# Performance work log

Hardware: AMD Instinct MI355X
Metric: run time of the kernel (lower is better)

Reference implementation:

```python
import jax, jax.numpy as jnp
import numpy as np

B, N, C, H = 2, 2048, 768, 12
D = C // H            # head_dim = 64
SCALE = D ** -0.5
QMAX_8 = 127.0        # int8 symmetric weights/activations (BIT_TYPE_W / BIT_TYPE_A)
LOG_QMAX = 15.0       # uint4 log-domain softmax (BIT_TYPE_S)


def setup_inputs() -> dict:
    key = jax.random.key(0)
    k0, k1, k2 = jax.random.split(key, 3)
    x = jax.random.normal(k0, (B, N, C), jnp.float32)
    w_qkv = jax.random.normal(k1, (3 * C, C), jnp.float32) * 0.02
    b_qkv = jnp.zeros((3 * C,), jnp.float32)
    w_out = jax.random.normal(k2, (C, C), jnp.float32) * 0.02
    b_out = jnp.zeros((C,), jnp.float32)
    return {"x": x, "w_qkv": w_qkv, "b_qkv": b_qkv, "w_out": w_out, "b_out": b_out}


def fake_quant_sym(t):
    """Symmetric per-tensor int8 fake-quantize (quantize->dequantize), STE for grads."""
    s = jnp.max(jnp.abs(t)) / QMAX_8 + 1e-8
    deq = jnp.clip(jnp.round(t / s), -QMAX_8, QMAX_8) * s
    return t + jax.lax.stop_gradient(deq - t)


def log_int_softmax(attn):
    """Log-int-softmax: softmax then 4-bit log2 quantization, attn_q = 2^{-round(-log2 p)}."""
    p = jax.nn.softmax(attn, axis=-1)
    lg = jnp.clip(jnp.round(-jnp.log2(jnp.maximum(p, 2.0 ** -24))), 0.0, LOG_QMAX)
    q = jnp.exp2(-lg)
    return p + jax.lax.stop_gradient(q - p)


def reference(x, w_qkv, b_qkv, w_out, b_out):
    # QLinear: fake-quantized weight GEMM
    qkv = x @ fake_quant_sym(w_qkv).T + b_qkv            # [B,N,3C]
    qkv = fake_quant_sym(qkv)                            # qact_qkv
    qkv = qkv.reshape(B, N, 3, H, D).transpose(2, 0, 3, 1, 4)  # [3,B,H,N,D]
    q, k, v = qkv[0], qkv[1], qkv[2]
    attn = jnp.einsum("bhnd,bhmd->bhnm", q, k) * SCALE   # [B,H,N,N]
    attn = fake_quant_sym(attn)                          # qact_attn
    p = log_int_softmax(attn)
    o = jnp.einsum("bhnm,bhmd->bhnd", p, v)              # [B,H,N,D]
    o = o.transpose(0, 2, 1, 3).reshape(B, N, C)
    out = o @ fake_quant_sym(w_out).T + b_out            # out_proj (QLinear)
    out = fake_quant_sym(out)                            # qact_out
    return out
```

## Files before the change

kernel.cpp:

```cpp
#include <hip/hip_runtime.h>

#define NB 2
#define NN 2048
#define NC 768
#define NH 12
#define ND 64
#define ROWS (NB * NN)
#define K3C (3 * NC)
#define NHEADS (NB * NH)
#define ATTN_SCALE 0.125f

typedef __attribute__((ext_vector_type(8))) short s16x8;
typedef __attribute__((ext_vector_type(4))) float f32x4;

__device__ __forceinline__ float qsc(const unsigned* u) {
    return __uint_as_float(*u) / 127.0f + 1e-8f;
}
__device__ __forceinline__ float fq(float t, float s) {
    return fminf(fmaxf(rintf(t / s), -127.0f), 127.0f) * s;
}
__device__ __forceinline__ float qcode(float t, float s) {
    return fminf(fmaxf(rintf(t / s), -127.0f), 127.0f);
}
__device__ __forceinline__ short bfbits(float f) {
    return (short)(__float_as_uint(f) >> 16);
}
__device__ __forceinline__ ushort bf_rne(float x) {
    unsigned u = __float_as_uint(x);
    return (ushort)((u + 0x7fffu + ((u >> 16) & 1u)) >> 16);
}

__global__ __launch_bounds__(256) void maxabs_kernel(const float* __restrict__ x,
                                                     long long n, unsigned* out) {
    float m = 0.0f;
    long long stride4 = (long long)gridDim.x * blockDim.x * 4;
    for (long long j = ((long long)blockIdx.x * blockDim.x + threadIdx.x) * 4; j < n; j += stride4) {
        float4 v = *(const float4*)(x + j);
        m = fmaxf(m, fmaxf(fmaxf(fabsf(v.x), fabsf(v.y)), fmaxf(fabsf(v.z), fabsf(v.w))));
    }
    for (int off = 32; off > 0; off >>= 1) m = fmaxf(m, __shfl_down(m, off, 64));
    __shared__ float sm[4];
    int lane = threadIdx.x & 63, w = threadIdx.x >> 6;
    if (lane == 0) sm[w] = m;
    __syncthreads();
    if (threadIdx.x == 0) {
        float mm = fmaxf(fmaxf(sm[0], sm[1]), fmaxf(sm[2], sm[3]));
        atomicMax(out, __float_as_uint(mm));
    }
}

__global__ __launch_bounds__(256) void quant_kernel(const float* in, float* out,
                                                    long long n, const unsigned* umax) {
    float s = qsc(umax);
    long long stride4 = (long long)gridDim.x * blockDim.x * 4;
    for (long long j = ((long long)blockIdx.x * blockDim.x + threadIdx.x) * 4; j < n; j += stride4) {
        float4 v = *(const float4*)(in + j);
        v.x = fq(v.x, s); v.y = fq(v.y, s); v.z = fq(v.z, s); v.w = fq(v.w, s);
        *(float4*)(out + j) = v;
    }
}

__global__ __launch_bounds__(256) void quantcodes_kernel(const float* __restrict__ in,
                                                         ushort* __restrict__ codes,
                                                         long long n,
                                                         const unsigned* __restrict__ umax) {
    float s = qsc(umax);
    long long stride8 = (long long)gridDim.x * blockDim.x * 8;
    for (long long j = ((long long)blockIdx.x * blockDim.x + threadIdx.x) * 8; j < n; j += stride8) {
        float4 a = *(const float4*)(in + j);
        float4 b = *(const float4*)(in + j + 4);
        s16x8 o;
        o[0] = bfbits(qcode(a.x, s)); o[1] = bfbits(qcode(a.y, s));
        o[2] = bfbits(qcode(a.z, s)); o[3] = bfbits(qcode(a.w, s));
        o[4] = bfbits(qcode(b.x, s)); o[5] = bfbits(qcode(b.y, s));
        o[6] = bfbits(qcode(b.z, s)); o[7] = bfbits(qcode(b.w, s));
        *(s16x8*)(codes + j) = o;
    }
}

__global__ __launch_bounds__(256) void split3_kernel(const float* __restrict__ in,
                                                     ushort* __restrict__ xs,
                                                     long long n) {
    long long stride8 = (long long)gridDim.x * blockDim.x * 8;
    for (long long j = ((long long)blockIdx.x * blockDim.x + threadIdx.x) * 8; j < n; j += stride8) {
        long long row = j / NC, col = j % NC;
        s16x8 h, m, l;
#pragma unroll
        for (int i = 0; i < 8; i += 4) {
            float4 v = *(const float4*)(in + j + i);
            float vv[4] = {v.x, v.y, v.z, v.w};
#pragma unroll
            for (int t = 0; t < 4; ++t) {
                ushort hb = bf_rne(vv[t]);
                float hf = __uint_as_float(((unsigned)hb) << 16);
                float r1 = vv[t] - hf;
                ushort mb = bf_rne(r1);
                float mf = __uint_as_float(((unsigned)mb) << 16);
                h[i + t] = (short)hb;
                m[i + t] = (short)mb;
                l[i + t] = (short)bf_rne(r1 - mf);
            }
        }
        ushort* dst = xs + row * (3 * NC) + col;
        *(s16x8*)(dst) = h;
        *(s16x8*)(dst + NC) = m;
        *(s16x8*)(dst + 2 * NC) = l;
    }
}

__global__ __launch_bounds__(256) void gemm3_mfma_kernel(const ushort* __restrict__ As,
                                                         const ushort* __restrict__ Bc,
                                                         const float* __restrict__ bias,
                                                         float* __restrict__ Cm, int Nn,
                                                         const unsigned* __restrict__ uB) {
    __shared__ ushort ah[128 * 64], am[128 * 64], al[128 * 64], bs[128 * 64];
    const float sB = qsc(uB);
    const int tid = threadIdx.x, l = tid & 63, w = tid >> 6;
    const int row0 = blockIdx.y * 128, col0 = blockIdx.x * 128;
    const int wr = w >> 1, wc = w & 1;
    f32x4 acc[4][4];
#pragma unroll
    for (int m = 0; m < 4; ++m)
#pragma unroll
        for (int n = 0; n < 4; ++n) acc[m][n] = (f32x4){0.f, 0.f, 0.f, 0.f};

    const int sr = tid >> 1, sh = (tid & 1) << 5;
    const int su = sh >> 3, s7 = sr & 7;

    for (int k0 = 0; k0 < NC; k0 += 64) {
        __syncthreads();
        {
            const ushort* ph = As + (size_t)(row0 + sr) * (3 * NC) + k0 + sh;
            ushort* dsts[3] = {ah + sr * 64, am + sr * 64, al + sr * 64};
#pragma unroll
            for (int pl = 0; pl < 3; ++pl) {
                const ushort* p = ph + pl * NC;
                s16x8 t0 = *(const s16x8*)(p),      t1 = *(const s16x8*)(p + 8);
                s16x8 t2 = *(const s16x8*)(p + 16), t3 = *(const s16x8*)(p + 24);
                ushort* d = dsts[pl];
                *(s16x8*)(d + (((su | 0) ^ s7) << 3)) = t0;
                *(s16x8*)(d + (((su | 1) ^ s7) << 3)) = t1;
                *(s16x8*)(d + (((su | 2) ^ s7) << 3)) = t2;
                *(s16x8*)(d + (((su | 3) ^ s7) << 3)) = t3;
            }
            const ushort* pb = Bc + (size_t)(col0 + sr) * NC + k0 + sh;
            s16x8 b0 = *(const s16x8*)(pb),      b1 = *(const s16x8*)(pb + 8);
            s16x8 b2 = *(const s16x8*)(pb + 16), b3 = *(const s16x8*)(pb + 24);
            ushort* brow = bs + sr * 64;
            *(s16x8*)(brow + (((su | 0) ^ s7) << 3)) = b0;
            *(s16x8*)(brow + (((su | 1) ^ s7) << 3)) = b1;
            *(s16x8*)(brow + (((su | 2) ^ s7) << 3)) = b2;
            *(s16x8*)(brow + (((su | 3) ^ s7) << 3)) = b3;
        }
        __syncthreads();
#pragma unroll
        for (int ks = 0; ks < 2; ++ks) {
            s16x8 bf[4];
#pragma unroll
            for (int n = 0; n < 4; ++n) {
                int br = wc * 64 + n * 16 + (l & 15);
                bf[n] = *(s16x8*)(bs + br * 64 + ((((ks << 2) + (l >> 4)) ^ (br & 7)) << 3));
            }
#pragma unroll
            for (int m = 0; m < 4; ++m) {
                int ar = wr * 64 + m * 16 + (l & 15);
                int ao = ar * 64 + ((((ks << 2) + (l >> 4)) ^ (ar & 7)) << 3);
                s16x8 af = *(s16x8*)(ah + ao);
                s16x8 mf_ = *(s16x8*)(am + ao);
                s16x8 ef = *(s16x8*)(al + ao);
#pragma unroll
                for (int n = 0; n < 4; ++n) {
                    acc[m][n] = __builtin_amdgcn_mfma_f32_16x16x32_bf16(af, bf[n], acc[m][n], 0, 0, 0);
                    acc[m][n] = __builtin_amdgcn_mfma_f32_16x16x32_bf16(mf_, bf[n], acc[m][n], 0, 0, 0);
                    acc[m][n] = __builtin_amdgcn_mfma_f32_16x16x32_bf16(ef, bf[n], acc[m][n], 0, 0, 0);
                }
            }
        }
    }
#pragma unroll
    for (int n = 0; n < 4; ++n) {
        int col = col0 + wc * 64 + n * 16 + (l & 15);
        float bv = bias[col];
#pragma unroll
        for (int m = 0; m < 4; ++m) {
            int grow = row0 + wr * 64 + m * 16 + ((l >> 4) << 2);
#pragma unroll
            for (int r = 0; r < 4; ++r)
                Cm[(size_t)(grow + r) * Nn + col] = fmaf(sB, acc[m][n][r], bv);
        }
    }
}

__device__ __forceinline__ void stage_k_tile(const ushort* __restrict__ src,
                                             ushort* lds, int tid) {
    int row = tid >> 2, u0 = (tid & 3) << 1, r7 = row & 7;
    const ushort* p = src + (size_t)row * K3C + (u0 << 3);
    s16x8 t0 = *(const s16x8*)(p);
    s16x8 t1 = *(const s16x8*)(p + 8);
    *(s16x8*)(lds + row * 64 + ((u0 ^ r7) << 3)) = t0;
    *(s16x8*)(lds + row * 64 + (((u0 | 1) ^ r7) << 3)) = t1;
}

__device__ __forceinline__ void stage_vT_tile(const ushort* __restrict__ src,
                                              ushort* lds, int tid) {
    int d = tid >> 2, j0 = (tid & 3) << 4;
    const ushort* p = src + (size_t)j0 * K3C + d;
    s16x8 a, b;
#pragma unroll
    for (int jj = 0; jj < 8; ++jj) a[jj] = (short)p[(size_t)jj * K3C];
#pragma unroll
    for (int jj = 0; jj < 8; ++jj) b[jj] = (short)p[(size_t)(8 + jj) * K3C];
    int u0 = j0 >> 3, d7 = d & 7;
    *(s16x8*)(lds + d * 64 + ((u0 ^ d7) << 3)) = a;
    *(s16x8*)(lds + d * 64 + (((u0 | 1) ^ d7) << 3)) = b;
}

__global__ __launch_bounds__(256) void attn_maxdot_kernel(const ushort* __restrict__ codes,
                                                          unsigned* __restrict__ umaxdot) {
    __shared__ ushort kt[64 * 64];
    __shared__ float red[4];
    int bh = blockIdx.y, b = bh / NH, h = bh % NH;
    int i0 = blockIdx.x * 64;
    int tid = threadIdx.x, l = tid & 63, w = tid >> 6;

    const ushort* qp = codes + (size_t)(b * NN + i0 + w * 16 + (l & 15)) * K3C + h * ND + ((l >> 4) << 3);
    s16x8 qf0 = *(const s16x8*)(qp);
    s16x8 qf1 = *(const s16x8*)(qp + 32);

    const ushort* kbase = codes + (size_t)(b * NN) * K3C + NC + h * ND;
    float md = 0.0f;
    for (int st = 0; st < NN / 64; ++st) {
        __syncthreads();
        stage_k_tile(kbase + (size_t)st * 64 * K3C, kt, tid);
        __syncthreads();
#pragma unroll
        for (int jt = 0; jt < 4; ++jt) {
            int row = (jt << 4) + (l & 15);
            f32x4 acc = {0.f, 0.f, 0.f, 0.f};
            s16x8 kf0 = *(s16x8*)(kt + row * 64 + ((((l >> 4)    ) ^ (row & 7)) << 3));
            s16x8 kf1 = *(s16x8*)(kt + row * 64 + ((((l >> 4) + 4) ^ (row & 7)) << 3));
            acc = __builtin_amdgcn_mfma_f32_16x16x32_bf16(qf0, kf0, acc, 0, 0, 0);
            acc = __builtin_amdgcn_mfma_f32_16x16x32_bf16(qf1, kf1, acc, 0, 0, 0);
#pragma unroll
            for (int r = 0; r < 4; ++r) md = fmaxf(md, fabsf(acc[r]));
        }
    }
    for (int m = 1; m < 64; m <<= 1) md = fmaxf(md, __shfl_xor(md, m, 64));
    if (l == 0) red[w] = md;
    __syncthreads();
    if (tid == 0)
        atomicMax(umaxdot, __float_as_uint(fmaxf(fmaxf(red[0], red[1]), fmaxf(red[2], red[3]))));
}

__global__ __launch_bounds__(256) void attn_fused_kernel(const ushort* __restrict__ codes,
                                                         const unsigned* __restrict__ uq,
                                                         const unsigned* __restrict__ umaxdot,
                                                         float* __restrict__ O) {
    __shared__ ushort kt[64 * 64];
    __shared__ ushort vt[64 * 64];
    __shared__ ushort ps[4][16 * 64];
    int bh = blockIdx.y, b = bh / NH, h = bh % NH;
    int i0 = blockIdx.x * 64;
    int tid = threadIdx.x, l = tid & 63, w = tid >> 6;
    float s = qsc(uq);
    float c = s * s * ATTN_SCALE;
    float sa = __uint_as_float(*umaxdot) * c / 127.0f + 1e-8f;
    float rr = c / sa;
    float kk = sa * 1.44269504088896340736f;

    const ushort* qp = codes + (size_t)(b * NN + i0 + w * 16 + (l & 15)) * K3C + h * ND + ((l >> 4) << 3);
    s16x8 qf0 = *(const s16x8*)(qp);
    s16x8 qf1 = *(const s16x8*)(qp + 32);

    const ushort* kbase = codes + (size_t)(b * NN) * K3C + NC + h * ND;
    const ushort* vbase = codes + (size_t)(b * NN) * K3C + 2 * NC + h * ND;

    float U[4] = {0.f, 0.f, 0.f, 0.f};
    for (int st = 0; st < NN / 64; ++st) {
        __syncthreads();
        stage_k_tile(kbase + (size_t)st * 64 * K3C, kt, tid);
        __syncthreads();
#pragma unroll
        for (int jt = 0; jt < 4; ++jt) {
            int row = (jt << 4) + (l & 15);
            f32x4 acc = {0.f, 0.f, 0.f, 0.f};
            s16x8 kf0 = *(s16x8*)(kt + row * 64 + ((((l >> 4)    ) ^ (row & 7)) << 3));
            s16x8 kf1 = *(s16x8*)(kt + row * 64 + ((((l >> 4) + 4) ^ (row & 7)) << 3));
            acc = __builtin_amdgcn_mfma_f32_16x16x32_bf16(qf0, kf0, acc, 0, 0, 0);
            acc = __builtin_amdgcn_mfma_f32_16x16x32_bf16(qf1, kf1, acc, 0, 0, 0);
#pragma unroll
            for (int r = 0; r < 4; ++r) {
                float m = rintf(acc[r] * rr);
                U[r] += exp2f(kk * m);
            }
        }
    }
#pragma unroll
    for (int r = 0; r < 4; ++r) {
        for (int msk = 1; msk < 16; msk <<= 1) U[r] += __shfl_xor(U[r], msk, 64);
    }
    float lu[4];
#pragma unroll
    for (int r = 0; r < 4; ++r) lu[r] = log2f(U[r]);

    f32x4 oacc[4];
#pragma unroll
    for (int dt = 0; dt < 4; ++dt) oacc[dt] = (f32x4){0.f, 0.f, 0.f, 0.f};
    ushort* myps = (ushort*)ps[w];
    for (int st = 0; st < NN / 64; ++st) {
        __syncthreads();
        stage_k_tile(kbase + (size_t)st * 64 * K3C, kt, tid);
        stage_vT_tile(vbase + (size_t)st * 64 * K3C, vt, tid);
        __syncthreads();
#pragma unroll
        for (int jt = 0; jt < 4; ++jt) {
            int row = (jt << 4) + (l & 15);
            f32x4 acc = {0.f, 0.f, 0.f, 0.f};
            s16x8 kf0 = *(s16x8*)(kt + row * 64 + ((((l >> 4)    ) ^ (row & 7)) << 3));
            s16x8 kf1 = *(s16x8*)(kt + row * 64 + ((((l >> 4) + 4) ^ (row & 7)) << 3));
            acc = __builtin_amdgcn_mfma_f32_16x16x32_bf16(qf0, kf0, acc, 0, 0, 0);
            acc = __builtin_amdgcn_mfma_f32_16x16x32_bf16(qf1, kf1, acc, 0, 0, 0);
#pragma unroll
            for (int r = 0; r < 4; ++r) {
                float m = rintf(acc[r] * rr);
                float tt = lu[r] - kk * m;
                float lg = fminf(fmaxf(rintf(tt), 0.0f), 15.0f);
                int lgi = (int)lg;
                ushort pbits = (ushort)((127 - lgi) << 7);
                int prow = ((l >> 4) << 2) + r;
                int j = (jt << 4) + (l & 15);
                int g = ((j >> 3) ^ (prow & 7)) ^ ((prow >> 3) << 2);
                myps[prow * 64 + (g << 3) + (j & 7)] = pbits;
            }
        }
#pragma unroll
        for (int kc = 0; kc < 2; ++kc) {
            int prow = l & 15;
            int gA = (((kc << 2) + (l >> 4)) ^ (prow & 7)) ^ ((prow >> 3) << 2);
            s16x8 pf = *(s16x8*)(myps + prow * 64 + (gA << 3));
#pragma unroll
            for (int dt = 0; dt < 4; ++dt) {
                int drow = (dt << 4) + (l & 15);
                s16x8 vf = *(s16x8*)(vt + drow * 64 + ((((kc << 2) + (l >> 4)) ^ (drow & 7)) << 3));
                oacc[dt] = __builtin_amdgcn_mfma_f32_16x16x32_bf16(pf, vf, oacc[dt], 0, 0, 0);
            }
        }
    }
#pragma unroll
    for (int dt = 0; dt < 4; ++dt)
#pragma unroll
        for (int r = 0; r < 4; ++r) {
            int orow = i0 + w * 16 + ((l >> 4) << 2) + r;
            O[(size_t)(b * NN + orow) * NC + h * ND + (dt << 4) + (l & 15)] = s * oacc[dt][r];
        }
}

extern "C" void kernel_launch(void* const* d_in, const int* in_sizes, int n_in,
                              void* d_out, int out_size, void* d_ws, size_t ws_size,
                              hipStream_t stream) {
    const float* x      = (const float*)d_in[0];
    const float* w_qkv  = (const float*)d_in[1];
    const float* b_qkv  = (const float*)d_in[2];
    const float* w_out  = (const float*)d_in[3];
    const float* b_out  = (const float*)d_in[4];
    float* out = (float*)d_out;

    char* ws = (char*)d_ws;
    unsigned* u = (unsigned*)ws;
    const size_t qkvB = (size_t)ROWS * K3C * 4;
    float*  qkv     = (float*)(ws + 256);
    float*  out_tmp = (float*)(ws + 256);
    ushort* woc     = (ushort*)(ws + 256 + 16 * 1024 * 1024);
    char*   codesRg = ws + 256 + qkvB;
    ushort* codes   = (ushort*)codesRg;
    ushort* xsplit  = (ushort*)codesRg;
    ushort* wqc     = (ushort*)d_out;

    hipMemsetAsync(u, 0, 64, stream);

    maxabs_kernel<<<512, 256, 0, stream>>>(w_qkv, (long long)K3C * NC, u + 0);
    maxabs_kernel<<<512, 256, 0, stream>>>(w_out, (long long)NC * NC, u + 1);
    quantcodes_kernel<<<512, 256, 0, stream>>>(w_qkv, wqc, (long long)K3C * NC, u + 0);

    split3_kernel<<<1024, 256, 0, stream>>>(x, xsplit, (long long)ROWS * NC);
    gemm3_mfma_kernel<<<dim3(K3C / 128, ROWS / 128), 256, 0, stream>>>(xsplit, wqc, b_qkv,
                                                                       qkv, K3C, u + 0);
    maxabs_kernel<<<1024, 256, 0, stream>>>(qkv, (long long)ROWS * K3C, u + 2);
    quantcodes_kernel<<<2048, 256, 0, stream>>>(qkv, codes, (long long)ROWS * K3C, u + 2);
    quantcodes_kernel<<<256, 256, 0, stream>>>(w_out, woc, (long long)NC * NC, u + 1);

    attn_maxdot_kernel<<<dim3(NN / 64, NHEADS), 256, 0, stream>>>(codes, u + 3);
    attn_fused_kernel<<<dim3(NN / 64, NHEADS), 256, 0, stream>>>(codes, u + 2, u + 3, out);

    split3_kernel<<<1024, 256, 0, stream>>>(out, xsplit, (long long)ROWS * NC);
    gemm3_mfma_kernel<<<dim3(NC / 128, ROWS / 128), 256, 0, stream>>>(xsplit, woc, b_out,
                                                                      out_tmp, NC, u + 1);
    maxabs_kernel<<<1024, 256, 0, stream>>>(out_tmp, (long long)ROWS * NC, u + 4);
    quant_kernel<<<1024, 256, 0, stream>>>(out_tmp, out, (long long)ROWS * NC, u + 4);
}
```

Baseline: 424.2 us.

## Fuse absmax into GEMM epilogue and transpose attention MFMA operands

Folds the per-tensor absmax reduction into the GEMM epilogue with wave shuffles and an atomicMax, which removes two full maxabs passes over the qkv and output tensors. The attention kernels swap the MFMA operand order so each lane holds a single query row's scores. That makes the softmax row sum a single scalar reduced with two shuffles, and the packed log-quantized probabilities are written with 8-byte LDS stores instead of scalar ones. V staging now uses coalesced vector global loads followed by scattered scalar LDS transposed writes, in place of strided global loads.

```diff
diff --git a/kernel.cpp b/kernel.cpp
--- a/kernel.cpp
+++ b/kernel.cpp
@@ -12,6 +12,7 @@
 
 typedef __attribute__((ext_vector_type(8))) short s16x8;
 typedef __attribute__((ext_vector_type(4))) float f32x4;
+typedef __attribute__((ext_vector_type(2))) unsigned int u32x2;
 
 __device__ __forceinline__ float qsc(const unsigned* u) {
     return __uint_as_float(*u) / 127.0f + 1e-8f;
@@ -112,8 +113,10 @@
                                                          const ushort* __restrict__ Bc,
                                                          const float* __restrict__ bias,
                                                          float* __restrict__ Cm, int Nn,
-                                                         const unsigned* __restrict__ uB) {
+                                                         const unsigned* __restrict__ uB,
+                                                         unsigned* __restrict__ uC) {
     __shared__ ushort ah[128 * 64], am[128 * 64], al[128 * 64], bs[128 * 64];
+    __shared__ float redmx[4];
     const float sB = qsc(uB);
     const int tid = threadIdx.x, l = tid & 63, w = tid >> 6;
     const int row0 = blockIdx.y * 128, col0 = blockIdx.x * 128;
@@ -177,6 +180,7 @@
             }
         }
     }
+    float mx = 0.0f;
 #pragma unroll
     for (int n = 0; n < 4; ++n) {
         int col = col0 + wc * 64 + n * 16 + (l & 15);
@@ -185,10 +189,18 @@
         for (int m = 0; m < 4; ++m) {
             int grow = row0 + wr * 64 + m * 16 + ((l >> 4) << 2);
 #pragma unroll
-            for (int r = 0; r < 4; ++r)
-                Cm[(size_t)(grow + r) * Nn + col] = fmaf(sB, acc[m][n][r], bv);
-        }
-    }
+            for (int r = 0; r < 4; ++r) {
+                float v = fmaf(sB, acc[m][n][r], bv);
+                Cm[(size_t)(grow + r) * Nn + col] = v;
+                mx = fmaxf(mx, fabsf(v));
+            }
+        }
+    }
+    for (int msk = 1; msk < 64; msk <<= 1) mx = fmaxf(mx, __shfl_xor(mx, msk, 64));
+    if (l == 0) redmx[w] = mx;
+    __syncthreads();
+    if (tid == 0)
+        atomicMax(uC, __float_as_uint(fmaxf(fmaxf(redmx[0], redmx[1]), fmaxf(redmx[2], redmx[3]))));
 }
 
 __device__ __forceinline__ void stage_k_tile(const ushort* __restrict__ src,
@@ -203,16 +215,21 @@
 
 __device__ __forceinline__ void stage_vT_tile(const ushort* __restrict__ src,
                                               ushort* lds, int tid) {
-    int d = tid >> 2, j0 = (tid & 3) << 4;
-    const ushort* p = src + (size_t)j0 * K3C + d;
-    s16x8 a, b;
-#pragma unroll
-    for (int jj = 0; jj < 8; ++jj) a[jj] = (short)p[(size_t)jj * K3C];
-#pragma unroll
-    for (int jj = 0; jj < 8; ++jj) b[jj] = (short)p[(size_t)(8 + jj) * K3C];
-    int u0 = j0 >> 3, d7 = d & 7;
-    *(s16x8*)(lds + d * 64 + ((u0 ^ d7) << 3)) = a;
-    *(s16x8*)(lds + d * 64 + (((u0 | 1) ^ d7) << 3)) = b;
+    int j = tid >> 2, d0 = (tid & 3) << 4;
+    const ushort* p = src + (size_t)j * K3C + d0;
+    s16x8 a = *(const s16x8*)(p);
+    s16x8 b = *(const s16x8*)(p + 8);
+    int jo = j >> 3, jl = j & 7;
+#pragma unroll
+    for (int t = 0; t < 8; ++t) {
+        int d = d0 + t;
+        lds[d * 64 + ((jo ^ (d & 7)) << 3) + jl] = (ushort)a[t];
+    }
+#pragma unroll
+    for (int t = 0; t < 8; ++t) {
+        int d = d0 + 8 + t;
+        lds[d * 64 + ((jo ^ (d & 7)) << 3) + jl] = (ushort)b[t];
+    }
 }
 
 __global__ __launch_bounds__(256) void attn_maxdot_kernel(const ushort* __restrict__ codes,
@@ -222,8 +239,9 @@
     int bh = blockIdx.y, b = bh / NH, h = bh % NH;
     int i0 = blockIdx.x * 64;
     int tid = threadIdx.x, l = tid & 63, w = tid >> 6;
-
-    const ushort* qp = codes + (size_t)(b * NN + i0 + w * 16 + (l & 15)) * K3C + h * ND + ((l >> 4) << 3);
+    int qr = l & 15, g = l >> 4;
+
+    const ushort* qp = codes + (size_t)(b * NN + i0 + w * 16 + qr) * K3C + h * ND + (g << 3);
     s16x8 qf0 = *(const s16x8*)(qp);
     s16x8 qf1 = *(const s16x8*)(qp + 32);
 
@@ -235,12 +253,12 @@
         __syncthreads();
 #pragma unroll
         for (int jt = 0; jt < 4; ++jt) {
-            int row = (jt << 4) + (l & 15);
+            int row = (jt << 4) + qr;
             f32x4 acc = {0.f, 0.f, 0.f, 0.f};
-            s16x8 kf0 = *(s16x8*)(kt + row * 64 + ((((l >> 4)    ) ^ (row & 7)) << 3));
-            s16x8 kf1 = *(s16x8*)(kt + row * 64 + ((((l >> 4) + 4) ^ (row & 7)) << 3));
-            acc = __builtin_amdgcn_mfma_f32_16x16x32_bf16(qf0, kf0, acc, 0, 0, 0);
-            acc = __builtin_amdgcn_mfma_f32_16x16x32_bf16(qf1, kf1, acc, 0, 0, 0);
+            s16x8 kf0 = *(s16x8*)(kt + row * 64 + (((g    ) ^ (row & 7)) << 3));
+            s16x8 kf1 = *(s16x8*)(kt + row * 64 + (((g + 4) ^ (row & 7)) << 3));
+            acc = __builtin_amdgcn_mfma_f32_16x16x32_bf16(kf0, qf0, acc, 0, 0, 0);
+            acc = __builtin_amdgcn_mfma_f32_16x16x32_bf16(kf1, qf1, acc, 0, 0, 0);
 #pragma unroll
             for (int r = 0; r < 4; ++r) md = fmaxf(md, fabsf(acc[r]));
         }
@@ -262,46 +280,43 @@
     int bh = blockIdx.y, b = bh / NH, h = bh % NH;
     int i0 = blockIdx.x * 64;
     int tid = threadIdx.x, l = tid & 63, w = tid >> 6;
+    int qr = l & 15, g = l >> 4;
     float s = qsc(uq);
-    float c = s * s * ATTN_SCALE;
-    float sa = __uint_as_float(*umaxdot) * c / 127.0f + 1e-8f;
-    float rr = c / sa;
+    float cf = s * s * ATTN_SCALE;
+    float sa = __uint_as_float(*umaxdot) * cf / 127.0f + 1e-8f;
+    float rr = cf / sa;
     float kk = sa * 1.44269504088896340736f;
 
-    const ushort* qp = codes + (size_t)(b * NN + i0 + w * 16 + (l & 15)) * K3C + h * ND + ((l >> 4) << 3);
+    const ushort* qp = codes + (size_t)(b * NN + i0 + w * 16 + qr) * K3C + h * ND + (g << 3);
     s16x8 qf0 = *(const s16x8*)(qp);
     s16x8 qf1 = *(const s16x8*)(qp + 32);
 
     const ushort* kbase = codes + (size_t)(b * NN) * K3C + NC + h * ND;
     const ushort* vbase = codes + (size_t)(b * NN) * K3C + 2 * NC + h * ND;
 
-    float U[4] = {0.f, 0.f, 0.f, 0.f};
+    float U = 0.0f;
     for (int st = 0; st < NN / 64; ++st) {
         __syncthreads();
         stage_k_tile(kbase + (size_t)st * 64 * K3C, kt, tid);
         __syncthreads();
 #pragma unroll
         for (int jt = 0; jt < 4; ++jt) {
-            int row = (jt << 4) + (l & 15);
+            int row = (jt << 4) + qr;
             f32x4 acc = {0.f, 0.f, 0.f, 0.f};
-            s16x8 kf0 = *(s16x8*)(kt + row * 64 + ((((l >> 4)    ) ^ (row & 7)) << 3));
-            s16x8 kf1 = *(s16x8*)(kt + row * 64 + ((((l >> 4) + 4) ^ (row & 7)) << 3));
-            acc = __builtin_amdgcn_mfma_f32_16x16x32_bf16(qf0, kf0, acc, 0, 0, 0);
-            acc = __builtin_amdgcn_mfma_f32_16x16x32_bf16(qf1, kf1, acc, 0, 0, 0);
+            s16x8 kf0 = *(s16x8*)(kt + row * 64 + (((g    ) ^ (row & 7)) << 3));
+            s16x8 kf1 = *(s16x8*)(kt + row * 64 + (((g + 4) ^ (row & 7)) << 3));
+            acc = __builtin_amdgcn_mfma_f32_16x16x32_bf16(kf0, qf0, acc, 0, 0, 0);
+            acc = __builtin_amdgcn_mfma_f32_16x16x32_bf16(kf1, qf1, acc, 0, 0, 0);
 #pragma unroll
             for (int r = 0; r < 4; ++r) {
                 float m = rintf(acc[r] * rr);
-                U[r] += exp2f(kk * m);
-            }
-        }
-    }
-#pragma unroll
-    for (int r = 0; r < 4; ++r) {
-        for (int msk = 1; msk < 16; msk <<= 1) U[r] += __shfl_xor(U[r], msk, 64);
-    }
-    float lu[4];
-#pragma unroll
-    for (int r = 0; r < 4; ++r) lu[r] = log2f(U[r]);
+                U += exp2f(kk * m);
+            }
+        }
+    }
+    U += __shfl_xor(U, 16, 64);
+    U += __shfl_xor(U, 32, 64);
+    float lu = log2f(U);
 
     f32x4 oacc[4];
 #pragma unroll
@@ -314,34 +329,32 @@
         __syncthreads();
 #pragma unroll
         for (int jt = 0; jt < 4; ++jt) {
-            int row = (jt << 4) + (l & 15);
+            int row = (jt << 4) + qr;
             f32x4 acc = {0.f, 0.f, 0.f, 0.f};
-            s16x8 kf0 = *(s16x8*)(kt + row * 64 + ((((l >> 4)    ) ^ (row & 7)) << 3));
-            s16x8 kf1 = *(s16x8*)(kt + row * 64 + ((((l >> 4) + 4) ^ (row & 7)) << 3));
-            acc = __builtin_amdgcn_mfma_f32_16x16x32_bf16(qf0, kf0, acc, 0, 0, 0);
-            acc = __builtin_amdgcn_mfma_f32_16x16x32_bf16(qf1, kf1, acc, 0, 0, 0);
+            s16x8 kf0 = *(s16x8*)(kt + row * 64 + (((g    ) ^ (row & 7)) << 3));
+            s16x8 kf1 = *(s16x8*)(kt + row * 64 + (((g + 4) ^ (row & 7)) << 3));
+            acc = __builtin_amdgcn_mfma_f32_16x16x32_bf16(kf0, qf0, acc, 0, 0, 0);
+            acc = __builtin_amdgcn_mfma_f32_16x16x32_bf16(kf1, qf1, acc, 0, 0, 0);
+            int lg[4];
 #pragma unroll
             for (int r = 0; r < 4; ++r) {
                 float m = rintf(acc[r] * rr);
-                float tt = lu[r] - kk * m;
-                float lg = fminf(fmaxf(rintf(tt), 0.0f), 15.0f);
-                int lgi = (int)lg;
-                ushort pbits = (ushort)((127 - lgi) << 7);
-                int prow = ((l >> 4) << 2) + r;
-                int j = (jt << 4) + (l & 15);
-                int g = ((j >> 3) ^ (prow & 7)) ^ ((prow >> 3) << 2);
-                myps[prow * 64 + (g << 3) + (j & 7)] = pbits;
-            }
+                float tt = lu - kk * m;
+                lg[r] = (int)fminf(fmaxf(rintf(tt), 0.0f), 15.0f);
+            }
+            unsigned w0 = (unsigned)(((127 - lg[0]) << 7) | ((127 - lg[1]) << 23));
+            unsigned w1 = (unsigned)(((127 - lg[2]) << 7) | ((127 - lg[3]) << 23));
+            int off = qr * 64 + (((jt << 4) + ((g >> 1) << 3)) ^ ((qr & 7) << 3)) + ((g & 1) << 2);
+            *(u32x2*)(myps + off) = (u32x2){w0, w1};
         }
 #pragma unroll
         for (int kc = 0; kc < 2; ++kc) {
-            int prow = l & 15;
-            int gA = (((kc << 2) + (l >> 4)) ^ (prow & 7)) ^ ((prow >> 3) << 2);
-            s16x8 pf = *(s16x8*)(myps + prow * 64 + (gA << 3));
+            int poff = qr * 64 + (((kc << 5) + (g << 3)) ^ ((qr & 7) << 3));
+            s16x8 pf = *(s16x8*)(myps + poff);
 #pragma unroll
             for (int dt = 0; dt < 4; ++dt) {
-                int drow = (dt << 4) + (l & 15);
-                s16x8 vf = *(s16x8*)(vt + drow * 64 + ((((kc << 2) + (l >> 4)) ^ (drow & 7)) << 3));
+                int drow = (dt << 4) + qr;
+                s16x8 vf = *(s16x8*)(vt + drow * 64 + ((((kc << 2) + g) ^ (drow & 7)) << 3));
                 oacc[dt] = __builtin_amdgcn_mfma_f32_16x16x32_bf16(pf, vf, oacc[dt], 0, 0, 0);
             }
         }
@@ -350,8 +363,8 @@
     for (int dt = 0; dt < 4; ++dt)
 #pragma unroll
         for (int r = 0; r < 4; ++r) {
-            int orow = i0 + w * 16 + ((l >> 4) << 2) + r;
-            O[(size_t)(b * NN + orow) * NC + h * ND + (dt << 4) + (l & 15)] = s * oacc[dt][r];
+            int orow = i0 + w * 16 + (g << 2) + r;
+            O[(size_t)(b * NN + orow) * NC + h * ND + (dt << 4) + qr] = s * oacc[dt][r];
         }
 }
 
@@ -384,8 +397,7 @@
 
     split3_kernel<<<1024, 256, 0, stream>>>(x, xsplit, (long long)ROWS * NC);
     gemm3_mfma_kernel<<<dim3(K3C / 128, ROWS / 128), 256, 0, stream>>>(xsplit, wqc, b_qkv,
-                                                                       qkv, K3C, u + 0);
-    maxabs_kernel<<<1024, 256, 0, stream>>>(qkv, (long long)ROWS * K3C, u + 2);
+                                                                       qkv, K3C, u + 0, u + 2);
     quantcodes_kernel<<<2048, 256, 0, stream>>>(qkv, codes, (long long)ROWS * K3C, u + 2);
     quantcodes_kernel<<<256, 256, 0, stream>>>(w_out, woc, (long long)NC * NC, u + 1);
 
@@ -394,7 +406,6 @@
 
     split3_kernel<<<1024, 256, 0, stream>>>(out, xsplit, (long long)ROWS * NC);
     gemm3_mfma_kernel<<<dim3(NC / 128, ROWS / 128), 256, 0, stream>>>(xsplit, woc, b_out,
-                                                                      out_tmp, NC, u + 1);
-    maxabs_kernel<<<1024, 256, 0, stream>>>(out_tmp, (long long)ROWS * NC, u + 4);
+                                                                      out_tmp, NC, u + 1, u + 4);
     quant_kernel<<<1024, 256, 0, stream>>>(out_tmp, out, (long long)ROWS * NC, u + 4);
 }
```

Measured after the change: 363.1 us. -14.4%, faster.
